# Performance work log

Measured on AMD Instinct MI355X. Metric: run time of the kernel, lower is better.

## Reference

```python
import jax, jax.numpy as jnp
import numpy as np

PAD = 39  # padding_value; output_dim = PAD + 1 = 40


def setup_inputs() -> dict:
    key = jax.random.key(0)
    k1, k2 = jax.random.split(key)
    x = jax.random.randint(k1, (256, 4096), 0, 101)          # unit ids in [0, 100]
    W = jax.random.normal(k2, (101, 40), dtype=jnp.float32)   # embedding table
    return {"x": x, "W": W}


def reference(x, W):
    # nn.Embedding(max_norm=1): looked-up rows are renormalized to L2 norm <= 1.
    rows = W[x]                                               # [B, L, D] gather
    norm = jnp.linalg.norm(rows, axis=-1, keepdims=True)
    scale = jax.lax.stop_gradient(jnp.minimum(1.0, 1.0 / jnp.maximum(norm, 1e-12)))
    probs = rows * scale                                      # [B, L, D]

    # labels = argmax over detached probs
    labels = jnp.argmax(jax.lax.stop_gradient(probs), axis=-1)  # [B, L] int

    # Batched unique_consecutive (run-length encode), fully vectorized:
    # keep[i, t] = True iff labels[i, t] starts a new run.
    B, L = labels.shape
    first = jnp.ones((B, 1), dtype=bool)
    change = labels[:, 1:] != labels[:, :-1]
    keep = jnp.concatenate([first, change], axis=1)           # [B, L] bool
    # inverse indices: which run each position belongs to (== torch return_inverse)
    inv = jnp.cumsum(keep.astype(labels.dtype), axis=1) - 1   # [B, L]

    # labels_ded: compacted run values, padded with PAD.
    rows_idx = jnp.broadcast_to(jnp.arange(B)[:, None], (B, L))
    labels_ded = jnp.full((B, L), PAD, dtype=labels.dtype).at[rows_idx, inv].set(labels)
    # (duplicate scatter indices within a run all write the same value)

    return probs, labels, labels_ded, inv
```

## Files before the change

kernel.cpp:

```cpp
#include <hip/hip_runtime.h>

static constexpr int Bn = 256;
static constexpr int Ln = 4096;
static constexpr int Dn = 40;
static constexpr int NU = 101;
static constexpr float PADF = 39.0f;
static constexpr int PROBS_BLOCKS = 2048;
static constexpr int TOTAL_BLOCKS = PROBS_BLOCKS + Bn;

__global__ __launch_bounds__(256) void fused_kernel(const int* __restrict__ x,
                                                    const float* __restrict__ W,
                                                    float* __restrict__ out) {
    __shared__ float sW[NU * Dn];
    __shared__ int slab[NU];
    __shared__ int wsum[4];

    float* probs  = out;
    float* labels = out + (size_t)Bn * Ln * Dn;
    float* ded    = labels + (size_t)Bn * Ln;
    float* inv    = ded + (size_t)Bn * Ln;

    const int tid = threadIdx.x;
    const int bid = blockIdx.x;

    if (bid >= Bn) {
        float4* sW4 = (float4*)sW;
        const float4* W4 = (const float4*)W;
        for (int i = tid; i < NU * Dn / 4; i += 256) sW4[i] = W4[i];
        __syncthreads();
        if (tid < NU) {
            float ss = 0.f;
#pragma unroll
            for (int d = 0; d < Dn; ++d) { float v = sW[tid * Dn + d]; ss += v * v; }
            float scale = fminf(1.0f, 1.0f / fmaxf(sqrtf(ss), 1e-12f));
#pragma unroll
            for (int d = 0; d < Dn; ++d) sW[tid * Dn + d] *= scale;
        }
        __syncthreads();

        const int total = Bn * Ln * 10;
        const int stride = PROBS_BLOCKS * 256;
        float4* out4 = (float4*)probs;
        for (int g = (bid - Bn) * 256 + tid; g < total; g += stride) {
            int p = g / 10;
            int c = g - p * 10;
            int u = x[p];
            out4[g] = sW4[u * 10 + c];
        }
    } else {
        if (tid < NU) {
            const float* wr = W + tid * Dn;
            float ss = 0.f;
#pragma unroll
            for (int d = 0; d < Dn; ++d) { float v = wr[d]; ss += v * v; }
            float scale = fminf(1.0f, 1.0f / fmaxf(sqrtf(ss), 1e-12f));
            float best = -3.4e38f; int bi = 0;
#pragma unroll
            for (int d = 0; d < Dn; ++d) {
                float v = wr[d] * scale;
                if (v > best) { best = v; bi = d; }
            }
            slab[tid] = bi;
        }
        __syncthreads();

        const int row = bid;
        const int* xr = x + row * Ln;
        const int t0 = tid * 16;

        int xv[16];
        const int4* xp = (const int4*)(xr + t0);
#pragma unroll
        for (int q = 0; q < 4; ++q) {
            int4 a = xp[q];
            xv[q * 4 + 0] = a.x; xv[q * 4 + 1] = a.y;
            xv[q * 4 + 2] = a.z; xv[q * 4 + 3] = a.w;
        }
        const int prevlab = (tid == 0) ? -1 : slab[xr[t0 - 1]];

        int lv[16]; int invloc[16];
        int run = prevlab; int cnt = 0;
#pragma unroll
        for (int j = 0; j < 16; ++j) {
            lv[j] = slab[xv[j]];
            cnt += (lv[j] != run) ? 1 : 0;
            invloc[j] = cnt;
            run = lv[j];
        }

        const int lane = tid & 63;
        const int wid = tid >> 6;
        int incl = cnt;
#pragma unroll
        for (int off = 1; off < 64; off <<= 1) {
            int v = __shfl_up(incl, off, 64);
            if (lane >= off) incl += v;
        }
        if (lane == 63) wsum[wid] = incl;
        __syncthreads();
        int waveoff = 0;
        for (int w = 0; w < wid; ++w) waveoff += wsum[w];
        const int excl = waveoff + incl - cnt;

        float* lrow = labels + row * Ln + t0;
        float* irow = inv + row * Ln + t0;
        float* drow = ded + row * Ln;

        float lb[16], iv[16];
#pragma unroll
        for (int j = 0; j < 16; ++j) {
            lb[j] = (float)lv[j];
            iv[j] = (float)(excl + invloc[j] - 1);
        }
#pragma unroll
        for (int q = 0; q < 4; ++q) {
            ((float4*)lrow)[q] = make_float4(lb[q*4], lb[q*4+1], lb[q*4+2], lb[q*4+3]);
            ((float4*)irow)[q] = make_float4(iv[q*4], iv[q*4+1], iv[q*4+2], iv[q*4+3]);
            ((float4*)(drow + t0))[q] = make_float4(PADF, PADF, PADF, PADF);
        }
        __syncthreads();

        run = prevlab; int c2 = 0;
#pragma unroll
        for (int j = 0; j < 16; ++j) {
            if (lv[j] != run) {
                drow[excl + c2] = (float)lv[j];
                ++c2;
            }
            run = lv[j];
        }
    }
}

extern "C" void kernel_launch(void* const* d_in, const int* in_sizes, int n_in,
                              void* d_out, int out_size, void* d_ws, size_t ws_size,
                              hipStream_t stream) {
    const int* x = (const int*)d_in[0];
    const float* W = (const float*)d_in[1];
    float* out = (float*)d_out;

    fused_kernel<<<TOTAL_BLOCKS, 256, 0, stream>>>(x, W, out);
}
```

Measured before the change: 43.87 us.

## Balance probs gather across all blocks and stage dedup row in shared memory

Reduces the grid to 2048 blocks. Each block writes a fixed contiguous chunk of the probs output, and the RLE blocks take a slightly smaller chunk after finishing their row work, so load is balanced with no separate tail of RLE blocks. Each block stages its x indices in shared memory so the gather reads x once per position, not once per float4. The labels_ded row is built in shared memory and written out with coalesced float4 stores, replacing a global pad fill followed by scattered writes. The cost is that shared memory is reused across phases with hand-computed offsets and there are extra barriers.

Result: faster. 37.53 us (-14.4%).

```diff
diff --git a/kernel.cpp b/kernel.cpp
--- a/kernel.cpp
+++ b/kernel.cpp
@@ -5,15 +5,26 @@
 static constexpr int Dn = 40;
 static constexpr int NU = 101;
 static constexpr float PADF = 39.0f;
-static constexpr int PROBS_BLOCKS = 2048;
-static constexpr int TOTAL_BLOCKS = PROBS_BLOCKS + Bn;
+
+static constexpr int NBLK = 2048;
+static constexpr int T_F4 = Bn * Ln * (Dn / 4);
+static constexpr int Q_PROBS = 5184;
+static constexpr int Q_RLE   = 4672;
+static_assert((NBLK - Bn) * Q_PROBS + Bn * Q_RLE == T_F4, "probs split must cover exactly");
+
+static constexpr int SMEM_BYTES = 18432;
 
 __global__ __launch_bounds__(256) void fused_kernel(const int* __restrict__ x,
                                                     const float* __restrict__ W,
                                                     float* __restrict__ out) {
-    __shared__ float sW[NU * Dn];
-    __shared__ int slab[NU];
-    __shared__ int wsum[4];
+    __shared__ __align__(16) char smem[SMEM_BYTES];
+    float4* sW4 = (float4*)smem;
+    float*  sW  = (float*)smem;
+    int*    sx  = (int*)(smem + 16160);
+    float*  sded  = (float*)smem;
+    float4* sded4 = (float4*)smem;
+    int*    slab  = (int*)(smem + 16384);
+    int*    wsum  = (int*)(smem + 16384 + 101 * 4);
 
     float* probs  = out;
     float* labels = out + (size_t)Bn * Ln * Dn;
@@ -23,31 +34,11 @@
     const int tid = threadIdx.x;
     const int bid = blockIdx.x;
 
-    if (bid >= Bn) {
-        float4* sW4 = (float4*)sW;
-        const float4* W4 = (const float4*)W;
-        for (int i = tid; i < NU * Dn / 4; i += 256) sW4[i] = W4[i];
-        __syncthreads();
-        if (tid < NU) {
-            float ss = 0.f;
-#pragma unroll
-            for (int d = 0; d < Dn; ++d) { float v = sW[tid * Dn + d]; ss += v * v; }
-            float scale = fminf(1.0f, 1.0f / fmaxf(sqrtf(ss), 1e-12f));
-#pragma unroll
-            for (int d = 0; d < Dn; ++d) sW[tid * Dn + d] *= scale;
-        }
-        __syncthreads();
+    int start, len;
+    if (bid < Bn) {
+        start = (NBLK - Bn) * Q_PROBS + bid * Q_RLE;
+        len = Q_RLE;
 
-        const int total = Bn * Ln * 10;
-        const int stride = PROBS_BLOCKS * 256;
-        float4* out4 = (float4*)probs;
-        for (int g = (bid - Bn) * 256 + tid; g < total; g += stride) {
-            int p = g / 10;
-            int c = g - p * 10;
-            int u = x[p];
-            out4[g] = sW4[u * 10 + c];
-        }
-    } else {
         if (tid < NU) {
             const float* wr = W + tid * Dn;
             float ss = 0.f;
@@ -61,6 +52,10 @@
                 if (v > best) { best = v; bi = d; }
             }
             slab[tid] = bi;
+        }
+        {
+            const float4 padv = make_float4(PADF, PADF, PADF, PADF);
+            for (int i = tid; i < Ln / 4; i += 256) sded4[i] = padv;
         }
         __syncthreads();
 
@@ -104,7 +99,6 @@
 
         float* lrow = labels + row * Ln + t0;
         float* irow = inv + row * Ln + t0;
-        float* drow = ded + row * Ln;
 
         float lb[16], iv[16];
 #pragma unroll
@@ -116,18 +110,51 @@
         for (int q = 0; q < 4; ++q) {
             ((float4*)lrow)[q] = make_float4(lb[q*4], lb[q*4+1], lb[q*4+2], lb[q*4+3]);
             ((float4*)irow)[q] = make_float4(iv[q*4], iv[q*4+1], iv[q*4+2], iv[q*4+3]);
-            ((float4*)(drow + t0))[q] = make_float4(PADF, PADF, PADF, PADF);
         }
-        __syncthreads();
 
         run = prevlab; int c2 = 0;
 #pragma unroll
         for (int j = 0; j < 16; ++j) {
             if (lv[j] != run) {
-                drow[excl + c2] = (float)lv[j];
+                sded[excl + c2] = (float)lv[j];
                 ++c2;
             }
             run = lv[j];
+        }
+        __syncthreads();
+        float4* drow4 = (float4*)(ded + row * Ln);
+        for (int i = tid; i < Ln / 4; i += 256) drow4[i] = sded4[i];
+        __syncthreads();
+    } else {
+        start = (bid - Bn) * Q_PROBS;
+        len = Q_PROBS;
+    }
+
+    {
+        const float4* W4 = (const float4*)W;
+        for (int i = tid; i < NU * Dn / 4; i += 256) sW4[i] = W4[i];
+        __syncthreads();
+        if (tid < NU) {
+            float ss = 0.f;
+#pragma unroll
+            for (int d = 0; d < Dn; ++d) { float v = sW[tid * Dn + d]; ss += v * v; }
+            float scale = fminf(1.0f, 1.0f / fmaxf(sqrtf(ss), 1e-12f));
+#pragma unroll
+            for (int d = 0; d < Dn; ++d) sW[tid * Dn + d] *= scale;
+        }
+        const int pbase = start / 10;
+        const int pend = (start + len - 1) / 10;
+        const int pcnt = pend - pbase + 1;
+        for (int i = tid; i < pcnt; i += 256) sx[i] = x[pbase + i];
+        __syncthreads();
+
+        float4* out4 = (float4*)probs;
+        const int end = start + len;
+        for (int idx = start + tid; idx < end; idx += 256) {
+            int p = idx / 10;
+            int c = idx - p * 10;
+            int u = sx[p - pbase];
+            out4[idx] = sW4[u * 10 + c];
         }
     }
 }
@@ -139,5 +166,5 @@
     const float* W = (const float*)d_in[1];
     float* out = (float*)d_out;
 
-    fused_kernel<<<TOTAL_BLOCKS, 256, 0, stream>>>(x, W, out);
+    fused_kernel<<<NBLK, 256, 0, stream>>>(x, W, out);
 }
```
